# Performance work log

Measured on AMD Instinct MI355X. Metric: run time of the kernel, lower is better.

## Reference

```python
import jax, jax.numpy as jnp
import numpy as np

SIZE = 512
NUM_HEADS = 8
HEAD_SIZE = SIZE // NUM_HEADS
EPS = 1e-5  # GroupNorm default eps


def setup_inputs() -> dict:
    key = jax.random.key(0)
    ks = jax.random.split(key, 8)
    B, T, D = 2, 2048, SIZE
    mk = lambda k: jax.random.normal(k, (D, D), dtype=jnp.float32) / D
    return {
        "x": jax.random.normal(ks[0], (B, T, D), dtype=jnp.float32),
        "W_Q": mk(ks[1]),
        "W_K": mk(ks[2]),
        "W_V": mk(ks[3]),
        "W_G": mk(ks[4]),
        "W_O": mk(ks[5]),
        "gn_weight": jnp.ones((D,), dtype=jnp.float32),
        "gn_bias": jnp.zeros((D,), dtype=jnp.float32),
    }


def _retention(x, W_Q, W_K, W_V):
    B, T, D = x.shape
    H, dh = NUM_HEADS, HEAD_SIZE
    # projections -> (B, H, T, dh)
    q = (x @ W_Q).reshape(B, T, H, dh).transpose(0, 2, 1, 3)
    k = (x @ W_K).reshape(B, T, H, dh).transpose(0, 2, 1, 3)
    v = (x @ W_V).reshape(B, T, H, dh).transpose(0, 2, 1, 3)
    # multi-scale per-head decay: gamma_h = 1 - 2^{-5-h}
    gammas = 1.0 - jnp.exp2(-5.0 - jnp.arange(H, dtype=jnp.float32))
    idx = jnp.arange(T)
    diff = (idx[:, None] - idx[None, :]).astype(jnp.float32)  # (T, T)
    causal = diff >= 0
    # D[h, n, m] = gamma_h^{n-m} for n >= m else 0
    decay = jnp.where(causal[None], jnp.exp(diff[None] * jnp.log(gammas)[:, None, None]), 0.0)
    scores = jnp.einsum("bhtd,bhsd->bhts", q, k) / jnp.sqrt(jnp.float32(dh))
    out = jnp.einsum("bhts,bhsd->bhtd", scores * decay[None], v)
    return out.transpose(0, 2, 1, 3).reshape(B, T, D)


def _group_norm(y, weight, bias):
    # GroupNorm(NUM_HEADS, SIZE) over flattened (B*T, SIZE)
    B, T, D = y.shape
    g = y.reshape(B * T, NUM_HEADS, HEAD_SIZE)
    mean = jnp.mean(g, axis=-1, keepdims=True)
    var = jnp.var(g, axis=-1, keepdims=True)
    g = (g - mean) / jnp.sqrt(var + EPS)
    g = g.reshape(B * T, D) * weight + bias
    return g.reshape(B, T, D)


def reference(x, W_Q, W_K, W_V, W_G, W_O, gn_weight, gn_bias):
    ret = _retention(x, W_Q, W_K, W_V)          # (B, T, D)
    normed = _group_norm(ret, gn_weight, gn_bias)  # (B, T, D)
    return jax.nn.silu(x @ W_G + normed) @ W_O
```

## Files before the change

kernel.cpp:

```cpp
#include <hip/hip_runtime.h>
#include <hip/hip_bf16.h>
#include <math.h>

#define DMODEL 512
#define T_SEQ 2048
#define NH 8
#define DH 64
#define M_ROWS 4096
#define LDST 72

typedef short s16x8 __attribute__((ext_vector_type(8)));
typedef float f32x4 __attribute__((ext_vector_type(4)));
typedef unsigned short u16x4 __attribute__((ext_vector_type(4)));

static __device__ __forceinline__ unsigned short f2bf(float f) {
  __hip_bfloat16 h = __float2bfloat16(f);
  return *(unsigned short*)&h;
}
static __device__ __forceinline__ float bf2f(unsigned short u) {
  union { unsigned int i; float f; } x; x.i = (unsigned int)u << 16; return x.f;
}
static __device__ __forceinline__ void gld16(void* lds, const void* g) {
  __builtin_amdgcn_global_load_lds(
      (const __attribute__((address_space(1))) unsigned int*)g,
      (__attribute__((address_space(3))) unsigned int*)lds, 16, 0, 0);
}

__global__ __launch_bounds__(256) void prep_k(
    const float* __restrict__ x, unsigned short* __restrict__ Xb,
    const float* __restrict__ W0, const float* __restrict__ W1,
    const float* __restrict__ W2, const float* __restrict__ W3,
    const float* __restrict__ W4, unsigned short* __restrict__ WT)
{
  __shared__ __align__(16) unsigned short buf[64 * LDST];
  const int bid = blockIdx.x, tid = threadIdx.x;
  if (bid < 1024) {
    const size_t i = ((size_t)bid * 256 + tid) * 8;
    float4 a = *(const float4*)&x[i];
    float4 b = *(const float4*)&x[i + 4];
    s16x8 o;
    o[0]=f2bf(a.x); o[1]=f2bf(a.y); o[2]=f2bf(a.z); o[3]=f2bf(a.w);
    o[4]=f2bf(b.x); o[5]=f2bf(b.y); o[6]=f2bf(b.z); o[7]=f2bf(b.w);
    *(s16x8*)&Xb[i] = o;
    return;
  }
  const int bid2 = bid - 1024;
  const int z = bid2 >> 6, rem = bid2 & 63;
  const int n0 = (rem & 7) * 64, k0 = (rem >> 3) * 64;
  const float* W = (z==0)?W0:(z==1)?W1:(z==2)?W2:(z==3)?W3:W4;
  #pragma unroll
  for (int r = 0; r < 4; ++r) {
    int idx = r * 256 + tid;
    int kr = idx >> 4, nc = idx & 15;
    float4 v = *(const float4*)&W[(size_t)(k0 + kr) * DMODEL + n0 + nc * 4];
    buf[(nc*4+0) * LDST + kr] = f2bf(v.x);
    buf[(nc*4+1) * LDST + kr] = f2bf(v.y);
    buf[(nc*4+2) * LDST + kr] = f2bf(v.z);
    buf[(nc*4+3) * LDST + kr] = f2bf(v.w);
  }
  __syncthreads();
  #pragma unroll
  for (int r = 0; r < 2; ++r) {
    int idx = r * 256 + tid;
    int nr = idx >> 3, c = idx & 7;
    *(s16x8*)&WT[((size_t)z * DMODEL + n0 + nr) * DMODEL + k0 + c * 8] =
        *(const s16x8*)&buf[nr * LDST + c * 8];
  }
}

__global__ __launch_bounds__(256) void mfma_gemm_k(
    const unsigned short* __restrict__ A, const unsigned short* __restrict__ BT,
    void* __restrict__ C0, void* __restrict__ C1,
    void* __restrict__ C2, void* __restrict__ C3, int nbf16)
{
  __shared__ __align__(16) unsigned short As[128 * 64];
  __shared__ __align__(16) unsigned short Bs[128 * 64];
  const int ng0 = blockIdx.x * 128;
  const int m0 = blockIdx.y * 128;
  const int z = ng0 >> 9, n0 = ng0 & 511;
  void* Cz = (z==0)?C0:(z==1)?C1:(z==2)?C2:C3;
  const int tid = threadIdx.x;
  const int wave = tid >> 6, lane = tid & 63;
  const int wm = wave >> 1, wn = wave & 1;
  const int n = lane & 15, quad = lane >> 4;

  int srow[4], scol[4];
  #pragma unroll
  for (int r = 0; r < 4; ++r) {
    int idx = r * 256 + tid;
    srow[r] = idx >> 3;
    scol[r] = ((idx & 7) ^ (srow[r] & 7)) * 8;
  }

  f32x4 acc[4][4];
  #pragma unroll
  for (int mi = 0; mi < 4; ++mi)
    #pragma unroll
    for (int ni = 0; ni < 4; ++ni) acc[mi][ni] = (f32x4){0.f,0.f,0.f,0.f};

  for (int k0 = 0; k0 < 512; k0 += 64) {
    #pragma unroll
    for (int r = 0; r < 4; ++r) {
      int idx = r * 256 + tid;
      gld16(&As[idx * 8], &A[(size_t)(m0 + srow[r]) * DMODEL + k0 + scol[r]]);
      gld16(&Bs[idx * 8], &BT[(size_t)(ng0 + srow[r]) * DMODEL + k0 + scol[r]]);
    }
    __syncthreads();
    #pragma unroll
    for (int kk = 0; kk < 2; ++kk) {
      s16x8 af[4], bf[4];
      #pragma unroll
      for (int mi = 0; mi < 4; ++mi) {
        int R = wm*64 + mi*16 + n, cc = (kk*4 + quad) ^ (n & 7);
        af[mi] = *(const s16x8*)&As[R * 64 + cc * 8];
      }
      #pragma unroll
      for (int ni = 0; ni < 4; ++ni) {
        int R = wn*64 + ni*16 + n, cc = (kk*4 + quad) ^ (n & 7);
        bf[ni] = *(const s16x8*)&Bs[R * 64 + cc * 8];
      }
      #pragma unroll
      for (int mi = 0; mi < 4; ++mi)
        #pragma unroll
        for (int ni = 0; ni < 4; ++ni)
          acc[mi][ni] = __builtin_amdgcn_mfma_f32_16x16x32_bf16(
              af[mi], bf[ni], acc[mi][ni], 0, 0, 0);
    }
    __syncthreads();
  }

  if (z < nbf16) {
    unsigned short* Cb = (unsigned short*)Cz;
    #pragma unroll
    for (int mi = 0; mi < 4; ++mi)
      #pragma unroll
      for (int ni = 0; ni < 4; ++ni)
        #pragma unroll
        for (int r = 0; r < 4; ++r)
          Cb[(size_t)(m0 + wm*64 + mi*16 + quad*4 + r) * DMODEL +
             n0 + wn*64 + ni*16 + n] = f2bf(acc[mi][ni][r]);
  } else {
    float* Cf = (float*)Cz;
    #pragma unroll
    for (int mi = 0; mi < 4; ++mi)
      #pragma unroll
      for (int ni = 0; ni < 4; ++ni)
        #pragma unroll
        for (int r = 0; r < 4; ++r)
          Cf[(size_t)(m0 + wm*64 + mi*16 + quad*4 + r) * DMODEL +
             n0 + wn*64 + ni*16 + n] = acc[mi][ni][r];
  }
}

__global__ __launch_bounds__(256) void ret_kv_k(
    const unsigned short* __restrict__ Kb, const unsigned short* __restrict__ Vb,
    float* __restrict__ AT)
{
  __shared__ __align__(16) unsigned short Kts[64 * LDST];
  __shared__ __align__(16) unsigned short Vts[64 * LDST];
  const int c = blockIdx.x, h = blockIdx.y, b = blockIdx.z;
  const int bh = b * NH + h;
  const int tid = threadIdx.x;
  const int wave = tid >> 6, lane = tid & 63;
  const int n = lane & 15, quad = lane >> 4;
  const size_t base = ((size_t)b * T_SEQ + (size_t)c * 64) * DMODEL + h * DH;
  const float lg = log2f(1.0f - exp2f(-5.0f - (float)h));

  #pragma unroll
  for (int r = 0; r < 2; ++r) {
    int idx = r * 256 + tid;
    int m = idx & 63, ch = idx >> 6;
    s16x8 kv = *(const s16x8*)&Kb[base + (size_t)m * DMODEL + ch * 8];
    s16x8 vv = *(const s16x8*)&Vb[base + (size_t)m * DMODEL + ch * 8];
    float sc = exp2f((float)(64 - m) * lg);
    #pragma unroll
    for (int e = 0; e < 8; ++e) {
      Kts[(ch * 8 + e) * LDST + m] = f2bf(bf2f(((unsigned short*)&kv)[e]) * sc);
      Vts[(ch * 8 + e) * LDST + m] = ((unsigned short*)&vv)[e];
    }
  }
  __syncthreads();

  f32x4 at[4];
  #pragma unroll
  for (int j = 0; j < 4; ++j) at[j] = (f32x4){0.f,0.f,0.f,0.f};
  #pragma unroll
  for (int kk = 0; kk < 2; ++kk) {
    s16x8 a = *(const s16x8*)&Vts[(wave*16 + n) * LDST + kk*32 + quad*8];
    #pragma unroll
    for (int j = 0; j < 4; ++j) {
      s16x8 bf = *(const s16x8*)&Kts[(j*16 + n) * LDST + kk*32 + quad*8];
      at[j] = __builtin_amdgcn_mfma_f32_16x16x32_bf16(a, bf, at[j], 0, 0, 0);
    }
  }
  float* Ab = AT + (((size_t)bh * 32 + c) << 12);
  #pragma unroll
  for (int j = 0; j < 4; ++j)
    #pragma unroll
    for (int r = 0; r < 4; ++r)
      Ab[(wave*16 + quad*4 + r) * 64 + j*16 + n] = at[j][r];
}

__global__ __launch_bounds__(256) void ret_scan_k(
    const float* __restrict__ AT, unsigned short* __restrict__ St)
{
  const int q = blockIdx.x, bh = blockIdx.y;
  const float lg = log2f(1.0f - exp2f(-5.0f - (float)(bh & 7)));
  const float g64 = exp2f(64.0f * lg);
  const size_t eoff = (size_t)q * 1024 + (size_t)threadIdx.x * 4;
  const float* Ab = AT + (((size_t)bh * 32) << 12) + eoff;
  unsigned short* Sb = St + (((size_t)bh * 32) << 12) + eoff;
  float4 S = make_float4(0.f, 0.f, 0.f, 0.f);
  float4 nxt = *(const float4*)Ab;
  for (int c = 0; c < 32; ++c) {
    float4 a = nxt;
    if (c < 31) nxt = *(const float4*)(Ab + ((size_t)(c + 1) << 12));
    u16x4 o;
    o[0] = f2bf(S.x); o[1] = f2bf(S.y); o[2] = f2bf(S.z); o[3] = f2bf(S.w);
    *(u16x4*)(Sb + ((size_t)c << 12)) = o;
    S.x = fmaf(g64, S.x, a.x); S.y = fmaf(g64, S.y, a.y);
    S.z = fmaf(g64, S.z, a.z); S.w = fmaf(g64, S.w, a.w);
  }
}

__global__ __launch_bounds__(256) void ret_o_k(
    const unsigned short* __restrict__ Qb, const unsigned short* __restrict__ Kb,
    const unsigned short* __restrict__ Vb, const unsigned short* __restrict__ St,
    float* __restrict__ RET)
{
  __shared__ __align__(16) unsigned short Qs[64 * LDST];
  __shared__ __align__(16) unsigned short Ks[64 * LDST];
  __shared__ __align__(16) unsigned short Vst[64 * LDST];
  __shared__ __align__(16) unsigned short Ss[64 * LDST];
  __shared__ __align__(16) unsigned short Ps[64 * LDST];
  const int c = blockIdx.x, h = blockIdx.y, b = blockIdx.z;
  const int bh = b * NH + h;
  const int tid = threadIdx.x;
  const int wave = tid >> 6, lane = tid & 63;
  const int n = lane & 15, quad = lane >> 4;
  const size_t base = ((size_t)b * T_SEQ + (size_t)c * 64) * DMODEL + h * DH;
  const unsigned short* Sg = St + (((size_t)bh * 32 + c) << 12);
  const float lg = log2f(1.0f - exp2f(-5.0f - (float)h));

  #pragma unroll
  for (int r = 0; r < 2; ++r) {
    int idx = r * 256 + tid;
    int i = idx >> 3, ch = idx & 7;
    *(s16x8*)&Qs[i * LDST + ch * 8] =
        *(const s16x8*)&Qb[base + (size_t)i * DMODEL + ch * 8];
    *(s16x8*)&Ks[i * LDST + ch * 8] =
        *(const s16x8*)&Kb[base + (size_t)i * DMODEL + ch * 8];
    *(s16x8*)&Ss[i * LDST + ch * 8] = *(const s16x8*)&Sg[i * 64 + ch * 8];
  }
  #pragma unroll
  for (int r = 0; r < 2; ++r) {
    int idx = r * 256 + tid;
    int m = idx & 63, ch = idx >> 6;
    s16x8 vv = *(const s16x8*)&Vb[base + (size_t)m * DMODEL + ch * 8];
    #pragma unroll
    for (int e = 0; e < 8; ++e)
      Vst[(ch * 8 + e) * LDST + m] = ((unsigned short*)&vv)[e];
  }
  __syncthreads();

  f32x4 s[4], u[4];
  #pragma unroll
  for (int j = 0; j < 4; ++j) {
    s[j] = (f32x4){0.f,0.f,0.f,0.f};
    u[j] = (f32x4){0.f,0.f,0.f,0.f};
  }
  #pragma unroll
  for (int kk = 0; kk < 2; ++kk) {
    s16x8 a = *(const s16x8*)&Qs[(wave*16 + n) * LDST + kk*32 + quad*8];
    #pragma unroll
    for (int j = 0; j < 4; ++j) {
      s16x8 bk = *(const s16x8*)&Ks[(j*16 + n) * LDST + kk*32 + quad*8];
      s[j] = __builtin_amdgcn_mfma_f32_16x16x32_bf16(a, bk, s[j], 0, 0, 0);
      s16x8 bs = *(const s16x8*)&Ss[(j*16 + n) * LDST + kk*32 + quad*8];
      u[j] = __builtin_amdgcn_mfma_f32_16x16x32_bf16(a, bs, u[j], 0, 0, 0);
    }
  }

  float rowf[4], colf[4];
  #pragma unroll
  for (int r = 0; r < 4; ++r) rowf[r] = exp2f((float)(wave*16 + quad*4 + r) * lg);
  #pragma unroll
  for (int j = 0; j < 4; ++j) colf[j] = exp2f(-(float)(j*16 + n) * lg);

  #pragma unroll
  for (int j = 0; j < 4; ++j)
    #pragma unroll
    for (int r = 0; r < 4; ++r) {
      int i = wave*16 + quad*4 + r, mcol = j*16 + n;
      float v = (mcol <= i) ? s[j][r] * 0.125f * rowf[r] * colf[j] : 0.0f;
      Ps[i * LDST + mcol] = f2bf(v);
    }
  __syncthreads();

  f32x4 acc[4];
  #pragma unroll
  for (int j = 0; j < 4; ++j) acc[j] = (f32x4){0.f,0.f,0.f,0.f};
  #pragma unroll
  for (int kk = 0; kk < 2; ++kk) {
    s16x8 a = *(const s16x8*)&Ps[(wave*16 + n) * LDST + kk*32 + quad*8];
    #pragma unroll
    for (int j = 0; j < 4; ++j) {
      s16x8 bf = *(const s16x8*)&Vst[(j*16 + n) * LDST + kk*32 + quad*8];
      acc[j] = __builtin_amdgcn_mfma_f32_16x16x32_bf16(a, bf, acc[j], 0, 0, 0);
    }
  }

  #pragma unroll
  for (int j = 0; j < 4; ++j)
    #pragma unroll
    for (int r = 0; r < 4; ++r) {
      int i = wave*16 + quad*4 + r;
      RET[((size_t)b * T_SEQ + (size_t)c * 64 + i) * DMODEL + h*DH + j*16 + n] =
          acc[j][r] + 0.125f * rowf[r] * u[j][r];
    }
}

__global__ __launch_bounds__(512) void gn_gate_k(
    const float* __restrict__ RET, const unsigned short* __restrict__ Gg,
    const float* __restrict__ gw, const float* __restrict__ gb,
    unsigned short* __restrict__ S)
{
  const int row = blockIdx.x;
  const int tid = threadIdx.x;
  const float r = RET[(size_t)row * DMODEL + tid];
  float sum = r, sq = r * r;
  #pragma unroll
  for (int off = 32; off > 0; off >>= 1) {
    sum += __shfl_xor(sum, off, 64);
    sq  += __shfl_xor(sq,  off, 64);
  }
  const float mean = sum * (1.0f / 64.0f);
  float var = sq * (1.0f / 64.0f) - mean * mean;
  var = fmaxf(var, 0.0f);
  const float rstd = rsqrtf(var + 1e-5f);
  const float normed = (r - mean) * rstd * gw[tid] + gb[tid];
  const float u = bf2f(Gg[(size_t)row * DMODEL + tid]) + normed;
  S[(size_t)row * DMODEL + tid] = f2bf(u / (1.0f + expf(-u)));
}

extern "C" void kernel_launch(void* const* d_in, const int* in_sizes, int n_in,
                              void* d_out, int out_size, void* d_ws, size_t ws_size,
                              hipStream_t stream) {
  const float* x   = (const float*)d_in[0];
  const float* WQ  = (const float*)d_in[1];
  const float* WK  = (const float*)d_in[2];
  const float* WV  = (const float*)d_in[3];
  const float* WG  = (const float*)d_in[4];
  const float* WO  = (const float*)d_in[5];
  const float* gnw = (const float*)d_in[6];
  const float* gnb = (const float*)d_in[7];
  float* out = (float*)d_out;

  char* ws = (char*)d_ws;
  unsigned short* Xb = (unsigned short*)(ws);
  unsigned short* Qb = (unsigned short*)(ws + 4  * (1<<20));
  unsigned short* Kb = (unsigned short*)(ws + 8  * (1<<20));
  unsigned short* Vb = (unsigned short*)(ws + 12 * (1<<20));
  unsigned short* G  = (unsigned short*)(ws + 16 * (1<<20));
  float* AT  = (float*)(ws + 24 * (1<<20));
  float* RET = AT;
  unsigned short* Sb = (unsigned short*)(ws + 32 * (1<<20));
  unsigned short* WT = (unsigned short*)(ws + 36 * (1<<20));
  unsigned short* St = (unsigned short*)(ws + 40 * (1<<20));
  (void)ws_size;

  prep_k<<<dim3(1024 + 320), 256, 0, stream>>>(x, Xb, WQ, WK, WV, WG, WO, WT);
  mfma_gemm_k<<<dim3(16, M_ROWS / 128), 256, 0, stream>>>(
      Xb, WT, Qb, Kb, Vb, G, 4);
  ret_kv_k<<<dim3(T_SEQ / 64, NH, 2), 256, 0, stream>>>(Kb, Vb, AT);
  ret_scan_k<<<dim3(4, 16), 256, 0, stream>>>(AT, St);
  ret_o_k<<<dim3(T_SEQ / 64, NH, 2), 256, 0, stream>>>(Qb, Kb, Vb, St, RET);
  gn_gate_k<<<dim3(M_ROWS), 512, 0, stream>>>(RET, G, gnw, gnb, Sb);
  mfma_gemm_k<<<dim3(4, M_ROWS / 128), 256, 0, stream>>>(
      Sb, WT + 4 * DMODEL * DMODEL, out, out, out, out, 0);
}
```

Measured before the change: 126.5 us.

## Fuse chunk-state scan into retention output kernel and GroupNorm-gate into output GEMM

Removes the separate scan kernel: each output block recomputes its inter-chunk state by serially accumulating all previous chunks' KV outer products with the decay factor, and blocks are launched in reverse chunk order so the longest scans start first. GroupNorm, the gate add and SiLU are folded into the A-tile load of the final GEMM, which drops the gn_gate kernel and its bf16 intermediate buffer. This saves two launches and intermediate round trips through global memory. In exchange the state reads grow quadratically with chunk count, and GN/SiLU is recomputed once per N-tile (4 times).

Result: slower. 155.5 us (+22.9%).

```diff
diff --git a/kernel.cpp b/kernel.cpp
--- a/kernel.cpp
+++ b/kernel.cpp
@@ -70,15 +70,15 @@
 
 __global__ __launch_bounds__(256) void mfma_gemm_k(
     const unsigned short* __restrict__ A, const unsigned short* __restrict__ BT,
-    void* __restrict__ C0, void* __restrict__ C1,
-    void* __restrict__ C2, void* __restrict__ C3, int nbf16)
+    unsigned short* __restrict__ C0, unsigned short* __restrict__ C1,
+    unsigned short* __restrict__ C2, unsigned short* __restrict__ C3)
 {
   __shared__ __align__(16) unsigned short As[128 * 64];
   __shared__ __align__(16) unsigned short Bs[128 * 64];
   const int ng0 = blockIdx.x * 128;
   const int m0 = blockIdx.y * 128;
   const int z = ng0 >> 9, n0 = ng0 & 511;
-  void* Cz = (z==0)?C0:(z==1)?C1:(z==2)?C2:C3;
+  unsigned short* Cz = (z==0)?C0:(z==1)?C1:(z==2)?C2:C3;
   const int tid = threadIdx.x;
   const int wave = tid >> 6, lane = tid & 63;
   const int wm = wave >> 1, wn = wave & 1;
@@ -129,27 +129,14 @@
     __syncthreads();
   }
 
-  if (z < nbf16) {
-    unsigned short* Cb = (unsigned short*)Cz;
-    #pragma unroll
-    for (int mi = 0; mi < 4; ++mi)
-      #pragma unroll
-      for (int ni = 0; ni < 4; ++ni)
-        #pragma unroll
-        for (int r = 0; r < 4; ++r)
-          Cb[(size_t)(m0 + wm*64 + mi*16 + quad*4 + r) * DMODEL +
-             n0 + wn*64 + ni*16 + n] = f2bf(acc[mi][ni][r]);
-  } else {
-    float* Cf = (float*)Cz;
-    #pragma unroll
-    for (int mi = 0; mi < 4; ++mi)
-      #pragma unroll
-      for (int ni = 0; ni < 4; ++ni)
-        #pragma unroll
-        for (int r = 0; r < 4; ++r)
-          Cf[(size_t)(m0 + wm*64 + mi*16 + quad*4 + r) * DMODEL +
-             n0 + wn*64 + ni*16 + n] = acc[mi][ni][r];
-  }
+  #pragma unroll
+  for (int mi = 0; mi < 4; ++mi)
+    #pragma unroll
+    for (int ni = 0; ni < 4; ++ni)
+      #pragma unroll
+      for (int r = 0; r < 4; ++r)
+        Cz[(size_t)(m0 + wm*64 + mi*16 + quad*4 + r) * DMODEL +
+           n0 + wn*64 + ni*16 + n] = f2bf(acc[mi][ni][r]);
 }
 
 __global__ __launch_bounds__(256) void ret_kv_k(
@@ -201,31 +188,9 @@
       Ab[(wave*16 + quad*4 + r) * 64 + j*16 + n] = at[j][r];
 }
 
-__global__ __launch_bounds__(256) void ret_scan_k(
-    const float* __restrict__ AT, unsigned short* __restrict__ St)
-{
-  const int q = blockIdx.x, bh = blockIdx.y;
-  const float lg = log2f(1.0f - exp2f(-5.0f - (float)(bh & 7)));
-  const float g64 = exp2f(64.0f * lg);
-  const size_t eoff = (size_t)q * 1024 + (size_t)threadIdx.x * 4;
-  const float* Ab = AT + (((size_t)bh * 32) << 12) + eoff;
-  unsigned short* Sb = St + (((size_t)bh * 32) << 12) + eoff;
-  float4 S = make_float4(0.f, 0.f, 0.f, 0.f);
-  float4 nxt = *(const float4*)Ab;
-  for (int c = 0; c < 32; ++c) {
-    float4 a = nxt;
-    if (c < 31) nxt = *(const float4*)(Ab + ((size_t)(c + 1) << 12));
-    u16x4 o;
-    o[0] = f2bf(S.x); o[1] = f2bf(S.y); o[2] = f2bf(S.z); o[3] = f2bf(S.w);
-    *(u16x4*)(Sb + ((size_t)c << 12)) = o;
-    S.x = fmaf(g64, S.x, a.x); S.y = fmaf(g64, S.y, a.y);
-    S.z = fmaf(g64, S.z, a.z); S.w = fmaf(g64, S.w, a.w);
-  }
-}
-
-__global__ __launch_bounds__(256) void ret_o_k(
+__global__ __launch_bounds__(256) void ret_o2_k(
     const unsigned short* __restrict__ Qb, const unsigned short* __restrict__ Kb,
-    const unsigned short* __restrict__ Vb, const unsigned short* __restrict__ St,
+    const unsigned short* __restrict__ Vb, const float* __restrict__ AT,
     float* __restrict__ RET)
 {
   __shared__ __align__(16) unsigned short Qs[64 * LDST];
@@ -233,14 +198,15 @@
   __shared__ __align__(16) unsigned short Vst[64 * LDST];
   __shared__ __align__(16) unsigned short Ss[64 * LDST];
   __shared__ __align__(16) unsigned short Ps[64 * LDST];
-  const int c = blockIdx.x, h = blockIdx.y, b = blockIdx.z;
+  const int c = (int)gridDim.x - 1 - (int)blockIdx.x;
+  const int h = blockIdx.y, b = blockIdx.z;
   const int bh = b * NH + h;
   const int tid = threadIdx.x;
   const int wave = tid >> 6, lane = tid & 63;
   const int n = lane & 15, quad = lane >> 4;
   const size_t base = ((size_t)b * T_SEQ + (size_t)c * 64) * DMODEL + h * DH;
-  const unsigned short* Sg = St + (((size_t)bh * 32 + c) << 12);
   const float lg = log2f(1.0f - exp2f(-5.0f - (float)h));
+  const float g64 = exp2f(64.0f * lg);
 
   #pragma unroll
   for (int r = 0; r < 2; ++r) {
@@ -250,7 +216,6 @@
         *(const s16x8*)&Qb[base + (size_t)i * DMODEL + ch * 8];
     *(s16x8*)&Ks[i * LDST + ch * 8] =
         *(const s16x8*)&Kb[base + (size_t)i * DMODEL + ch * 8];
-    *(s16x8*)&Ss[i * LDST + ch * 8] = *(const s16x8*)&Sg[i * 64 + ch * 8];
   }
   #pragma unroll
   for (int r = 0; r < 2; ++r) {
@@ -260,6 +225,41 @@
     #pragma unroll
     for (int e = 0; e < 8; ++e)
       Vst[(ch * 8 + e) * LDST + m] = ((unsigned short*)&vv)[e];
+  }
+
+  const float* Ac = AT + (((size_t)bh * 32) << 12) + (size_t)tid * 16;
+  float4 S0 = {0,0,0,0}, S1 = S0, S2 = S0, S3 = S0;
+  if (c > 0) {
+    float4 n0 = *(const float4*)(Ac + 0);
+    float4 n1 = *(const float4*)(Ac + 4);
+    float4 n2 = *(const float4*)(Ac + 8);
+    float4 n3 = *(const float4*)(Ac + 12);
+    for (int cp = 0; cp < c; ++cp) {
+      float4 a0 = n0, a1 = n1, a2 = n2, a3 = n3;
+      if (cp + 1 < c) {
+        const float* p = Ac + ((size_t)(cp + 1) << 12);
+        n0 = *(const float4*)(p + 0);  n1 = *(const float4*)(p + 4);
+        n2 = *(const float4*)(p + 8);  n3 = *(const float4*)(p + 12);
+      }
+      S0.x = fmaf(g64, S0.x, a0.x); S0.y = fmaf(g64, S0.y, a0.y);
+      S0.z = fmaf(g64, S0.z, a0.z); S0.w = fmaf(g64, S0.w, a0.w);
+      S1.x = fmaf(g64, S1.x, a1.x); S1.y = fmaf(g64, S1.y, a1.y);
+      S1.z = fmaf(g64, S1.z, a1.z); S1.w = fmaf(g64, S1.w, a1.w);
+      S2.x = fmaf(g64, S2.x, a2.x); S2.y = fmaf(g64, S2.y, a2.y);
+      S2.z = fmaf(g64, S2.z, a2.z); S2.w = fmaf(g64, S2.w, a2.w);
+      S3.x = fmaf(g64, S3.x, a3.x); S3.y = fmaf(g64, S3.y, a3.y);
+      S3.z = fmaf(g64, S3.z, a3.z); S3.w = fmaf(g64, S3.w, a3.w);
+    }
+  }
+  {
+    const int d2 = tid >> 2, d1b = (tid & 3) * 16;
+    s16x8 lo, hi;
+    lo[0]=f2bf(S0.x); lo[1]=f2bf(S0.y); lo[2]=f2bf(S0.z); lo[3]=f2bf(S0.w);
+    lo[4]=f2bf(S1.x); lo[5]=f2bf(S1.y); lo[6]=f2bf(S1.z); lo[7]=f2bf(S1.w);
+    hi[0]=f2bf(S2.x); hi[1]=f2bf(S2.y); hi[2]=f2bf(S2.z); hi[3]=f2bf(S2.w);
+    hi[4]=f2bf(S3.x); hi[5]=f2bf(S3.y); hi[6]=f2bf(S3.z); hi[7]=f2bf(S3.w);
+    *(s16x8*)&Ss[d2 * LDST + d1b] = lo;
+    *(s16x8*)&Ss[d2 * LDST + d1b + 8] = hi;
   }
   __syncthreads();
 
@@ -320,27 +320,108 @@
     }
 }
 
-__global__ __launch_bounds__(512) void gn_gate_k(
+__global__ __launch_bounds__(256) void out_gemm_k(
     const float* __restrict__ RET, const unsigned short* __restrict__ Gg,
-    const float* __restrict__ gw, const float* __restrict__ gb,
-    unsigned short* __restrict__ S)
+    const float* __restrict__ gnw, const float* __restrict__ gnb,
+    const unsigned short* __restrict__ BT, float* __restrict__ out)
 {
-  const int row = blockIdx.x;
+  __shared__ __align__(16) unsigned short As[128 * 64];
+  __shared__ __align__(16) unsigned short Bs[128 * 64];
+  const int n0 = blockIdx.x * 128;
+  const int m0 = blockIdx.y * 128;
   const int tid = threadIdx.x;
-  const float r = RET[(size_t)row * DMODEL + tid];
-  float sum = r, sq = r * r;
-  #pragma unroll
-  for (int off = 32; off > 0; off >>= 1) {
-    sum += __shfl_xor(sum, off, 64);
-    sq  += __shfl_xor(sq,  off, 64);
-  }
-  const float mean = sum * (1.0f / 64.0f);
-  float var = sq * (1.0f / 64.0f) - mean * mean;
-  var = fmaxf(var, 0.0f);
-  const float rstd = rsqrtf(var + 1e-5f);
-  const float normed = (r - mean) * rstd * gw[tid] + gb[tid];
-  const float u = bf2f(Gg[(size_t)row * DMODEL + tid]) + normed;
-  S[(size_t)row * DMODEL + tid] = f2bf(u / (1.0f + expf(-u)));
+  const int wave = tid >> 6, lane = tid & 63;
+  const int wm = wave >> 1, wn = wave & 1;
+  const int n = lane & 15, quad = lane >> 4;
+  const int arow = tid >> 1, ahalf = tid & 1;
+
+  int srow[4], scol[4];
+  #pragma unroll
+  for (int r = 0; r < 4; ++r) {
+    int idx = r * 256 + tid;
+    srow[r] = idx >> 3;
+    scol[r] = ((idx & 7) ^ (srow[r] & 7)) * 8;
+  }
+
+  f32x4 acc[4][4];
+  #pragma unroll
+  for (int mi = 0; mi < 4; ++mi)
+    #pragma unroll
+    for (int ni = 0; ni < 4; ++ni) acc[mi][ni] = (f32x4){0.f,0.f,0.f,0.f};
+
+  for (int k0 = 0; k0 < 512; k0 += 64) {
+    #pragma unroll
+    for (int r = 0; r < 4; ++r) {
+      int idx = r * 256 + tid;
+      gld16(&Bs[idx * 8], &BT[(size_t)(n0 + srow[r]) * DMODEL + k0 + scol[r]]);
+    }
+    {
+      const float* Rp = &RET[(size_t)(m0 + arow) * DMODEL + k0 + ahalf * 32];
+      float vals[32];
+      #pragma unroll
+      for (int q = 0; q < 8; ++q) {
+        float4 v = *(const float4*)(Rp + q * 4);
+        vals[q*4+0]=v.x; vals[q*4+1]=v.y; vals[q*4+2]=v.z; vals[q*4+3]=v.w;
+      }
+      float sum = 0.f, sq = 0.f;
+      #pragma unroll
+      for (int e = 0; e < 32; ++e) { sum += vals[e]; sq = fmaf(vals[e], vals[e], sq); }
+      sum += __shfl_xor(sum, 1);
+      sq  += __shfl_xor(sq, 1);
+      const float mean = sum * (1.0f / 64.0f);
+      float var = sq * (1.0f / 64.0f) - mean * mean;
+      var = fmaxf(var, 0.0f);
+      const float rstd = rsqrtf(var + 1e-5f);
+      const unsigned short* Gp = &Gg[(size_t)(m0 + arow) * DMODEL + k0 + ahalf * 32];
+      const float* wp = &gnw[k0 + ahalf * 32];
+      const float* bp = &gnb[k0 + ahalf * 32];
+      #pragma unroll
+      for (int cc = 0; cc < 4; ++cc) {
+        s16x8 gv = *(const s16x8*)(Gp + cc * 8);
+        s16x8 o;
+        #pragma unroll
+        for (int e = 0; e < 8; ++e) {
+          int col = cc * 8 + e;
+          float normed = (vals[col] - mean) * rstd * wp[col] + bp[col];
+          float uu = bf2f(((unsigned short*)&gv)[e]) + normed;
+          o[e] = f2bf(uu / (1.0f + expf(-uu)));
+        }
+        int chg = ahalf * 4 + cc;
+        *(s16x8*)&As[arow * 64 + (chg ^ (arow & 7)) * 8] = o;
+      }
+    }
+    __syncthreads();
+    #pragma unroll
+    for (int kk = 0; kk < 2; ++kk) {
+      s16x8 af[4], bf[4];
+      #pragma unroll
+      for (int mi = 0; mi < 4; ++mi) {
+        int R = wm*64 + mi*16 + n, cc = (kk*4 + quad) ^ (n & 7);
+        af[mi] = *(const s16x8*)&As[R * 64 + cc * 8];
+      }
+      #pragma unroll
+      for (int ni = 0; ni < 4; ++ni) {
+        int R = wn*64 + ni*16 + n, cc = (kk*4 + quad) ^ (n & 7);
+        bf[ni] = *(const s16x8*)&Bs[R * 64 + cc * 8];
+      }
+      #pragma unroll
+      for (int mi = 0; mi < 4; ++mi)
+        #pragma unroll
+        for (int ni = 0; ni < 4; ++ni)
+          acc[mi][ni] = __builtin_amdgcn_mfma_f32_16x16x32_bf16(
+              af[mi], bf[ni], acc[mi][ni], 0, 0, 0);
+    }
+    __syncthreads();
+  }
+
+  #pragma unroll
+  for (int mi = 0; mi < 4; ++mi)
+    #pragma unroll
+    for (int ni = 0; ni < 4; ++ni)
+      #pragma unroll
+      for (int r = 0; r < 4; ++r)
+        out[(size_t)(m0 + wm*64 + mi*16 + quad*4 + r) * DMODEL +
+            n0 + wn*64 + ni*16 + n] = acc[mi][ni][r];
 }
 
 extern "C" void kernel_launch(void* const* d_in, const int* in_sizes, int n_in,
@@ -363,19 +444,15 @@
   unsigned short* Vb = (unsigned short*)(ws + 12 * (1<<20));
   unsigned short* G  = (unsigned short*)(ws + 16 * (1<<20));
   float* AT  = (float*)(ws + 24 * (1<<20));
-  float* RET = AT;
-  unsigned short* Sb = (unsigned short*)(ws + 32 * (1<<20));
-  unsigned short* WT = (unsigned short*)(ws + 36 * (1<<20));
-  unsigned short* St = (unsigned short*)(ws + 40 * (1<<20));
+  float* RET = (float*)(ws + 32 * (1<<20));
+  unsigned short* WT = (unsigned short*)(ws + 40 * (1<<20));
   (void)ws_size;
 
   prep_k<<<dim3(1024 + 320), 256, 0, stream>>>(x, Xb, WQ, WK, WV, WG, WO, WT);
   mfma_gemm_k<<<dim3(16, M_ROWS / 128), 256, 0, stream>>>(
-      Xb, WT, Qb, Kb, Vb, G, 4);
+      Xb, WT, Qb, Kb, Vb, G);
   ret_kv_k<<<dim3(T_SEQ / 64, NH, 2), 256, 0, stream>>>(Kb, Vb, AT);
-  ret_scan_k<<<dim3(4, 16), 256, 0, stream>>>(AT, St);
-  ret_o_k<<<dim3(T_SEQ / 64, NH, 2), 256, 0, stream>>>(Qb, Kb, Vb, St, RET);
-  gn_gate_k<<<dim3(M_ROWS), 512, 0, stream>>>(RET, G, gnw, gnb, Sb);
-  mfma_gemm_k<<<dim3(4, M_ROWS / 128), 256, 0, stream>>>(
-      Sb, WT + 4 * DMODEL * DMODEL, out, out, out, out, 0);
-}
+  ret_o2_k<<<dim3(T_SEQ / 64, NH, 2), 256, 0, stream>>>(Qb, Kb, Vb, AT, RET);
+  out_gemm_k<<<dim3(4, M_ROWS / 128), 256, 0, stream>>>(
+      RET, G, gnw, gnb, WT + 4 * DMODEL * DMODEL, out);
+}
```
